# Kernel tuning notes

Hardware: AMD Instinct MI355X
Metric: run time of the kernel (lower is better)

## Reference

```python
import jax, jax.numpy as jnp
import numpy as np
from jax import lax

ANCHOR_AREAS = (128.0**2, 256.0**2, 512.0**2)
ASPECT_RATIOS = (0.5, 1.0, 2.0)
STRIDE = 32.0                      # resnet backbone: get_orig_stat maps fm -> input via x*32
PRE_NMS_TOP_N = 2000
POST_NMS_TOP_N = 100
NMS_IOU_T = 0.7
SCORE_T = 0.1
MIN_SCALE = 0.01
BBOX_XFORM_CLIP = float(np.log(1000.0 / 16.0))


def make_anchors(H, W):
    # anchors laid out in (H, W, A) order to match the offset permutation below
    sizes = []
    for area in ANCHOR_AREAS:
        for r in ASPECT_RATIOS:          # aspect_ratio = w / h
            sizes.append((np.sqrt(area * r), np.sqrt(area / r)))
    sizes = jnp.asarray(np.asarray(sizes, dtype=np.float32))  # [A, 2] (w, h)
    cy = (jnp.arange(H, dtype=jnp.float32) + 0.5) * STRIDE
    cx = (jnp.arange(W, dtype=jnp.float32) + 0.5) * STRIDE
    cyg, cxg = jnp.meshgrid(cy, cx, indexing='ij')             # [H, W]
    cxg = cxg[:, :, None]
    cyg = cyg[:, :, None]
    w = sizes[:, 0]
    h = sizes[:, 1]
    anchors = jnp.stack([cxg - w / 2, cyg - h / 2, cxg + w / 2, cyg + h / 2], axis=-1)
    return anchors.reshape(-1, 4)                              # [H*W*A, 4] xyxy


def decode_boxes(anchors, offsets):
    # anchors [N,4], offsets [B,N,4] (tx, ty, tw, th) -> boxes [B,N,4] xyxy
    wa = anchors[:, 2] - anchors[:, 0]
    ha = anchors[:, 3] - anchors[:, 1]
    cxa = anchors[:, 0] + 0.5 * wa
    cya = anchors[:, 1] + 0.5 * ha
    tx, ty = offsets[..., 0], offsets[..., 1]
    tw = jnp.minimum(offsets[..., 2], BBOX_XFORM_CLIP)
    th = jnp.minimum(offsets[..., 3], BBOX_XFORM_CLIP)
    px = tx * wa + cxa
    py = ty * ha + cya
    pw = jnp.exp(tw) * wa
    ph = jnp.exp(th) * ha
    return jnp.stack([px - pw / 2, py - ph / 2, px + pw / 2, py + ph / 2], axis=-1)


def box_iou(a, b):
    area_a = (a[:, 2] - a[:, 0]) * (a[:, 3] - a[:, 1])
    area_b = (b[:, 2] - b[:, 0]) * (b[:, 3] - b[:, 1])
    lt = jnp.maximum(a[:, None, :2], b[None, :, :2])
    rb = jnp.minimum(a[:, None, 2:], b[None, :, 2:])
    wh = jnp.clip(rb - lt, 0.0)
    inter = wh[..., 0] * wh[..., 1]
    return inter / (area_a[:, None] + area_b[None, :] - inter + 1e-9)


def nms_single(boxes, scores):
    # boxes [P,4] sorted by descending score; invalid entries carry score -1
    P = boxes.shape[0]
    iou = box_iou(boxes, boxes)
    idx = jnp.arange(P)

    def body(i, keep):
        sup = (iou[i] > NMS_IOU_T) & (idx > i)
        return jnp.where(keep[i], keep & (~sup), keep)

    keep = lax.stop_gradient(lax.fori_loop(0, P, body, scores > 0.0))
    kept_scores = jnp.where(keep, scores, -1.0)
    top_s, top_i = lax.top_k(kept_scores, POST_NMS_TOP_N)
    return boxes[top_i], top_s


def rpn_forward(features, W1, b1, W2, b2, W3, b3):
    B, Cin, H, W = features.shape
    A = W3.shape[0]
    # 3x3 sliding conv + ReLU
    t = lax.conv_general_dilated(
        features, W1, window_strides=(1, 1), padding='SAME',
        dimension_numbers=('NCHW', 'OIHW', 'NCHW'))
    t = jax.nn.relu(t + b1[None, :, None, None])
    # 1x1 sibling heads as channel contractions
    offs = jnp.einsum('bchw,oc->bohw', t, W2) + b2[None, :, None, None]   # [B, A*4, H, W]
    logits = jnp.einsum('bchw,oc->bohw', t, W3) + b3[None, :, None, None]  # [B, A, H, W]
    # reorder to per-anchor layout (H, W, A)
    offs = offs.reshape(B, A, 4, H, W).transpose(0, 3, 4, 1, 2).reshape(B, -1, 4)
    scores = jax.nn.sigmoid(logits.transpose(0, 2, 3, 1).reshape(B, -1))  # [B, N]
    anchors = make_anchors(H, W)
    boxes = decode_boxes(anchors, offs)                                    # [B, N, 4]
    # clip to image boundary (handle_cross_boundary_boxes during testing)
    img_w, img_h = W * STRIDE, H * STRIDE
    boxes = jnp.stack([
        jnp.clip(boxes[..., 0], 0.0, img_w),
        jnp.clip(boxes[..., 1], 0.0, img_h),
        jnp.clip(boxes[..., 2], 0.0, img_w),
        jnp.clip(boxes[..., 3], 0.0, img_h)], axis=-1)
    # score-threshold + min-scale filtering
    bw = boxes[..., 2] - boxes[..., 0]
    bh = boxes[..., 3] - boxes[..., 1]
    valid = (scores >= SCORE_T) & (bw > MIN_SCALE * img_w) & (bh > MIN_SCALE * img_h)
    masked = jnp.where(valid, scores, -1.0)
    # pre-NMS top-k, then per-image NMS + post-NMS top-n
    top_s, top_i = lax.top_k(masked, PRE_NMS_TOP_N)                        # [B, P]
    top_boxes = jnp.take_along_axis(boxes, top_i[..., None], axis=1)       # [B, P, 4]
    out_boxes, out_scores = jax.vmap(nms_single)(top_boxes, top_s)
    return out_boxes, out_scores                                           # [B,100,4], [B,100]


def setup_inputs() -> dict:
    key = jax.random.key(0)
    ks = jax.random.split(key, 4)
    B, Cin, H, W = 8, 1024, 50, 50
    A = 9
    C = 512
    return {
        'features': jax.random.normal(ks[0], (B, Cin, H, W), jnp.float32),
        'W1': jax.random.normal(ks[1], (C, Cin, 3, 3), jnp.float32) * 0.01,
        'b1': jnp.zeros((C,), jnp.float32),
        'W2': jax.random.normal(ks[2], (A * 4, C), jnp.float32) * 0.01,
        'b2': jnp.zeros((A * 4,), jnp.float32),
        'W3': jax.random.normal(ks[3], (A, C), jnp.float32) * 0.01,
        'b3': jnp.zeros((A,), jnp.float32),
    }


def reference(features, W1, b1, W2, b2, W3, b3):
    return rpn_forward(features, W1, b1, W2, b2, W3, b3)
```

## Files before the change

kernel.cpp:

```cpp
#include <hip/hip_runtime.h>
#include <cstdint>

#define NB 8
#define CIN 1024
#define HDIM 50
#define WDIM 50
#define COUT 512
#define NA 9
#define NANCH (HDIM*WDIM*NA)
#define PRE_N 2000
#define POST_N 100

typedef __attribute__((ext_vector_type(8))) short bf16x8;
typedef __attribute__((ext_vector_type(4))) float f32x4;
typedef __attribute__((ext_vector_type(16))) float f32x16;
typedef __attribute__((ext_vector_type(8))) unsigned short ushort8v;

constexpr size_t TPLANE    = 20578304;
constexpr size_t OFF_TPH   = 0;
constexpr size_t OFF_TPL   = 20578304;
constexpr size_t OFF_BOXES = 41156608;
constexpr size_t OFF_KEYS  = 44036608;
constexpr size_t OFF_TBOX  = 45476608;
constexpr size_t OFF_TS    = 45732608;
constexpr size_t OFF_SUP   = 45796608;
constexpr size_t QDIM      = 2976;
constexpr size_t PLSTRIDE  = QDIM * 8;
constexpr size_t PPLANE    = 48758784;
constexpr size_t OFF_PH    = 49892864;
constexpr size_t OFF_PL    = OFF_PH + PPLANE;
constexpr size_t WPLANE    = 9437184;
constexpr size_t OFF_WH    = 147410432;
constexpr size_t OFF_WL    = OFF_WH + WPLANE;

__device__ __forceinline__ void split2bf16(float v, unsigned short &hi, unsigned short &lo) {
    unsigned int u = __float_as_uint(v);
    unsigned int r = u + 0x7FFFu + ((u >> 16) & 1u);
    hi = (unsigned short)(r >> 16);
    float hf = __uint_as_float(((unsigned int)hi) << 16);
    float lf = v - hf;
    unsigned int u2 = __float_as_uint(lf);
    unsigned int r2 = u2 + 0x7FFFu + ((u2 >> 16) & 1u);
    lo = (unsigned short)(r2 >> 16);
}

__device__ __forceinline__ void gl_lds(const unsigned short* g, unsigned short* l) {
    __builtin_amdgcn_global_load_lds(
        (const __attribute__((address_space(1))) unsigned int*)(const void*)g,
        (__attribute__((address_space(3))) unsigned int*)(void*)l,
        16, 0, 0);
}

__global__ __launch_bounds__(256) void prep_all(const float* __restrict__ f,
                                                const float* __restrict__ W1,
                                                unsigned short* __restrict__ Ph,
                                                unsigned short* __restrict__ Pl,
                                                unsigned short* __restrict__ Wh,
                                                unsigned short* __restrict__ Wl) {
    int blk = blockIdx.x;
    if (blk < 5952) {
        int id = blk * 256 + threadIdx.x;
        int q = id % (int)QDIM; int r = id / (int)QDIM;
        int cic = r % 64; int b = r / 64;
        int pp = q - 53;
        int rr = pp / 52, cc = pp - rr * 52;
        int h = rr - 1, w = cc - 1;
        bool inb = (pp >= 0) && (pp < 2704) && (h >= 0) && (h < HDIM) && (w >= 0) && (w < WDIM);
        ushort8v hv0, lv0, hv1, lv1;
#pragma unroll
        for (int j = 0; j < 16; ++j) {
            float v = 0.f;
            if (inb) v = f[(((size_t)b * CIN + cic * 16 + j) * HDIM + h) * WDIM + w];
            unsigned short hi, lo;
            split2bf16(v, hi, lo);
            if (j < 8) { hv0[j] = hi; lv0[j] = lo; }
            else       { hv1[j - 8] = hi; lv1[j - 8] = lo; }
        }
        size_t b0 = ((size_t)((b * 64 + cic) * 2 + 0)) * PLSTRIDE + (size_t)q * 8;
        size_t b1 = ((size_t)((b * 64 + cic) * 2 + 1)) * PLSTRIDE + (size_t)q * 8;
        *(ushort8v*)&Ph[b0] = hv0;
        *(ushort8v*)&Ph[b1] = hv1;
        *(ushort8v*)&Pl[b0] = lv0;
        *(ushort8v*)&Pl[b1] = lv1;
    } else {
        int id = (blk - 5952) * 256 + threadIdx.x;
        int co = id % 64; int r = id / 64;
        int cic = r % 64; int cot = r / 64;
        int cog = cot * 64 + co;
        const float* src = W1 + ((size_t)cog * CIN + cic * 16) * 9;
        float v[144];
#pragma unroll
        for (int i = 0; i < 36; ++i) {
            float4 x = ((const float4*)src)[i];
            v[i * 4 + 0] = x.x; v[i * 4 + 1] = x.y; v[i * 4 + 2] = x.z; v[i * 4 + 3] = x.w;
        }
#pragma unroll
        for (int tap = 0; tap < 9; ++tap) {
            ushort8v hv0, lv0, hv1, lv1;
#pragma unroll
            for (int j = 0; j < 16; ++j) {
                unsigned short hi, lo;
                split2bf16(v[j * 9 + tap], hi, lo);
                if (j < 8) { hv0[j] = hi; lv0[j] = lo; }
                else       { hv1[j - 8] = hi; lv1[j - 8] = lo; }
            }
            size_t base = (((size_t)(cot * 64 + cic) * 9 + tap) * 2) * 512;
            *(ushort8v*)&Wh[base + co * 8]       = hv0;
            *(ushort8v*)&Wh[base + 512 + co * 8] = hv1;
            *(ushort8v*)&Wl[base + co * 8]       = lv0;
            *(ushort8v*)&Wl[base + 512 + co * 8] = lv1;
        }
    }
}

__global__ __launch_bounds__(256, 2) void conv_mfma(const unsigned short* __restrict__ FPh,
                                                    const unsigned short* __restrict__ FPl,
                                                    const unsigned short* __restrict__ WPh,
                                                    const unsigned short* __restrict__ WPl,
                                                    const float* __restrict__ b1,
                                                    unsigned short* __restrict__ Tph,
                                                    unsigned short* __restrict__ Tpl) {
    __shared__ unsigned short sA[2][2][3072];
    __shared__ unsigned short sB[2][9216];

    int blk = blockIdx.x;
    int cot = blk & 7;
    int ptile = (blk >> 3) % 11;
    int b = blk / 88;
    int co0 = cot * 64;
    int P0 = 32 + ptile * 256;

    int t = threadIdx.x, wv = t >> 6, ln = t & 63;
    int lm = ln & 31, lk = ln >> 5;

    f32x16 acc[2][2];
#pragma unroll
    for (int jm = 0; jm < 2; ++jm)
#pragma unroll
        for (int jn = 0; jn < 2; ++jn)
#pragma unroll
            for (int rg = 0; rg < 16; ++rg) acc[jm][jn][rg] = 0.f;

#pragma unroll 1
    for (int cic = 0; cic < 64; ++cic) {
        __syncthreads();
#pragma unroll
        for (int k = 0; k < 15; ++k) {
            int id = wv * 15 + k;
            if (id < 24) {
                int hl = id / 12, lkc = (id / 6) & 1, s = id % 6;
                const unsigned short* pl = hl ? FPl : FPh;
                const unsigned short* src = pl
                    + ((size_t)((b * 64 + cic) * 2 + lkc)) * PLSTRIDE
                    + (size_t)P0 * 8 + s * 512 + ln * 8;
                gl_lds(src, &sA[hl][lkc][s * 512]);
            } else {
                int j = id - 24;
                int hl = j / 18, s = j % 18;
                const unsigned short* pl = hl ? WPl : WPh;
                const unsigned short* src = pl + (size_t)(cot * 64 + cic) * 9216 + s * 512 + ln * 8;
                gl_lds(src, &sB[hl][s * 512]);
            }
        }
        __syncthreads();

#pragma unroll
        for (int tap = 0; tap < 9; ++tap) {
            const int kh = tap / 3, kw = tap % 3;
            const int dlt = (kh - 1) * 52 + (kw - 1);
            bf16x8 a[2][2], bb[2][2];
#pragma unroll
            for (int jm = 0; jm < 2; ++jm) {
                int e = (wv * 2 + jm) * 32 + lm + dlt + 53;
                int ad = e * 8;
                a[jm][0] = *(const bf16x8*)&sA[0][lk][ad];
                a[jm][1] = *(const bf16x8*)&sA[1][lk][ad];
            }
#pragma unroll
            for (int jn = 0; jn < 2; ++jn) {
                int bd = tap * 1024 + lk * 512 + (jn * 32 + lm) * 8;
                bb[jn][0] = *(const bf16x8*)&sB[0][bd];
                bb[jn][1] = *(const bf16x8*)&sB[1][bd];
            }
#pragma unroll
            for (int jm = 0; jm < 2; ++jm)
#pragma unroll
                for (int jn = 0; jn < 2; ++jn) {
                    acc[jm][jn] = __builtin_amdgcn_mfma_f32_32x32x16_bf16(a[jm][0], bb[jn][0], acc[jm][jn], 0, 0, 0);
                    acc[jm][jn] = __builtin_amdgcn_mfma_f32_32x32x16_bf16(a[jm][0], bb[jn][1], acc[jm][jn], 0, 0, 0);
                    acc[jm][jn] = __builtin_amdgcn_mfma_f32_32x32x16_bf16(a[jm][1], bb[jn][0], acc[jm][jn], 0, 0, 0);
                }
        }
    }

#pragma unroll
    for (int jn = 0; jn < 2; ++jn) {
        int co = co0 + jn * 32 + lm;
        float bv = b1[co];
#pragma unroll
        for (int jm = 0; jm < 2; ++jm) {
#pragma unroll
            for (int rg = 0; rg < 16; ++rg) {
                int mrow = (rg & 3) + 8 * (rg >> 2) + 4 * lk;
                int pp = P0 + (wv * 2 + jm) * 32 + mrow;
                int rr = pp / 52, cc = pp - rr * 52;
                int h = rr - 1, w = cc - 1;
                if ((unsigned)h < HDIM && (unsigned)w < WDIM) {
                    float v = fmaxf(acc[jm][jn][rg] + bv, 0.f);
                    unsigned short hi, lo;
                    split2bf16(v, hi, lo);
                    int px = b * 2500 + h * 50 + w;
                    size_t sa = (((((size_t)(px >> 7) * 16 + (co >> 5)) * 8 + ((px >> 4) & 7)) * 4
                                  + ((co >> 3) & 3)) * 16 + (px & 15)) * 8 + (co & 7);
                    Tph[sa] = hi;
                    Tpl[sa] = lo;
                }
            }
        }
    }
}

__global__ __launch_bounds__(256) void proj_decode_mfma(const unsigned short* __restrict__ Tph,
                                                        const unsigned short* __restrict__ Tpl,
                                                        const float* __restrict__ W2,
                                                        const float* __restrict__ b2,
                                                        const float* __restrict__ W3,
                                                        const float* __restrict__ b3,
                                                        float* __restrict__ boxes,
                                                        unsigned long long* __restrict__ keys) {
    __shared__ unsigned short sTh[4096], sTl[4096];
    __shared__ unsigned short sWh[1536], sWl[1536];
    __shared__ float pout[128 * 46];

    int blk = blockIdx.x;
    int px0 = blk * 128;
    int t = threadIdx.x, wv = t >> 6, ln = t & 63;
    int lm = ln & 15, q = ln >> 4;

    f32x4 acc[2][3];
#pragma unroll
    for (int jm = 0; jm < 2; ++jm)
#pragma unroll
        for (int nf = 0; nf < 3; ++nf) acc[jm][nf] = (f32x4){0.f, 0.f, 0.f, 0.f};

#pragma unroll 1
    for (int cc16 = 0; cc16 < 16; ++cc16) {
        __syncthreads();
        size_t base = ((size_t)blk * 16 + cc16) * 4096;
        if (wv == 0) {
#pragma unroll
            for (int s = 0; s < 4; ++s) gl_lds(Tph + base + s * 512 + ln * 8, &sTh[s * 512]);
        } else if (wv == 1) {
#pragma unroll
            for (int s = 4; s < 8; ++s) gl_lds(Tph + base + s * 512 + ln * 8, &sTh[s * 512]);
        } else if (wv == 2) {
#pragma unroll
            for (int s = 0; s < 4; ++s) gl_lds(Tpl + base + s * 512 + ln * 8, &sTl[s * 512]);
        } else {
#pragma unroll
            for (int s = 4; s < 8; ++s) gl_lds(Tpl + base + s * 512 + ln * 8, &sTl[s * 512]);
        }
        int c0 = cc16 * 32;
        for (int idx = t; idx < 1536; idx += 256) {
            int o = idx >> 5, ci = idx & 31;
            float v = 0.f;
            if (o < 36) v = W2[o * 512 + c0 + ci];
            else if (o < 45) v = W3[(o - 36) * 512 + c0 + ci];
            unsigned short hi, lo;
            split2bf16(v, hi, lo);
            int ad = (((o >> 4) * 4 + (ci >> 3)) * 16 + (o & 15)) * 8 + (ci & 7);
            sWh[ad] = hi; sWl[ad] = lo;
        }
        __syncthreads();

        bf16x8 a[2][2], bb[3][2];
#pragma unroll
        for (int jm = 0; jm < 2; ++jm) {
            int mf = wv * 2 + jm;
            int ad = ((mf * 4 + q) * 16 + lm) * 8;
            a[jm][0] = *(const bf16x8*)&sTh[ad];
            a[jm][1] = *(const bf16x8*)&sTl[ad];
        }
#pragma unroll
        for (int nf = 0; nf < 3; ++nf) {
            int ad = ((nf * 4 + q) * 16 + lm) * 8;
            bb[nf][0] = *(const bf16x8*)&sWh[ad];
            bb[nf][1] = *(const bf16x8*)&sWl[ad];
        }
#pragma unroll
        for (int jm = 0; jm < 2; ++jm)
#pragma unroll
            for (int nf = 0; nf < 3; ++nf) {
                acc[jm][nf] = __builtin_amdgcn_mfma_f32_16x16x32_bf16(a[jm][0], bb[nf][0], acc[jm][nf], 0, 0, 0);
                acc[jm][nf] = __builtin_amdgcn_mfma_f32_16x16x32_bf16(a[jm][0], bb[nf][1], acc[jm][nf], 0, 0, 0);
                acc[jm][nf] = __builtin_amdgcn_mfma_f32_16x16x32_bf16(a[jm][1], bb[nf][0], acc[jm][nf], 0, 0, 0);
            }
    }
    __syncthreads();
#pragma unroll
    for (int jm = 0; jm < 2; ++jm)
#pragma unroll
        for (int nf = 0; nf < 3; ++nf) {
            int o = nf * 16 + lm;
            if (o < 45) {
                float bias = (o < 36) ? b2[o] : b3[o - 36];
#pragma unroll
                for (int rg = 0; rg < 4; ++rg) {
                    int pxl = (wv * 2 + jm) * 16 + q * 4 + rg;
                    pout[pxl * 46 + o] = acc[jm][nf][rg] + bias;
                }
            }
        }
    __syncthreads();

    const float AW[9] = {90.50966799187809f, 128.0f, 181.01933598375618f,
                         181.01933598375618f, 256.0f, 362.03867196751236f,
                         362.03867196751236f, 512.0f, 724.0773439350247f};
    const float AH[9] = {181.01933598375618f, 128.0f, 90.50966799187809f,
                         362.03867196751236f, 256.0f, 181.01933598375618f,
                         724.0773439350247f, 512.0f, 362.03867196751236f};
    const float CLIPV = 4.135166556742356f;
    const float IMG = 1600.0f;

    for (int it = t; it < 128 * 9; it += 256) {
        int pxl = it / 9, a = it - pxl * 9;
        int pxg = px0 + pxl;
        if (pxg >= 20000) continue;
        int b = pxg / 2500, rem = pxg % 2500;
        int h = rem / 50, w = rem % 50;

        float tx = pout[pxl * 46 + a * 4 + 0];
        float ty = pout[pxl * 46 + a * 4 + 1];
        float tw = pout[pxl * 46 + a * 4 + 2];
        float th = pout[pxl * 46 + a * 4 + 3];
        float lg = pout[pxl * 46 + 36 + a];

        float s = 1.0f / (1.0f + expf(-lg));

        float cx = ((float)w + 0.5f) * 32.0f;
        float cy = ((float)h + 0.5f) * 32.0f;
        float x1a = cx - 0.5f * AW[a];
        float x2a = cx + 0.5f * AW[a];
        float y1a = cy - 0.5f * AH[a];
        float y2a = cy + 0.5f * AH[a];
        float waf = x2a - x1a;
        float haf = y2a - y1a;
        float cxa = x1a + 0.5f * waf;
        float cya = y1a + 0.5f * haf;

        float twc = tw < CLIPV ? tw : CLIPV;
        float thc = th < CLIPV ? th : CLIPV;
        float pxc = tx * waf + cxa;
        float pyc = ty * haf + cya;
        float pw  = expf(twc) * waf;
        float ph  = expf(thc) * haf;

        float x1 = pxc - 0.5f * pw;
        float y1 = pyc - 0.5f * ph;
        float x2 = pxc + 0.5f * pw;
        float y2 = pyc + 0.5f * ph;
        x1 = fminf(fmaxf(x1, 0.f), IMG);
        y1 = fminf(fmaxf(y1, 0.f), IMG);
        x2 = fminf(fmaxf(x2, 0.f), IMG);
        y2 = fminf(fmaxf(y2, 0.f), IMG);

        float bw = x2 - x1, bh = y2 - y1;
        bool valid = (s >= 0.1f) && (bw > 16.0f) && (bh > 16.0f);
        float m = valid ? s : -1.0f;

        int idx = (h * WDIM + w) * NA + a;
        size_t gi = (size_t)b * NANCH + idx;
        ((float4*)boxes)[gi] = make_float4(x1, y1, x2, y2);
        unsigned int u = __float_as_uint(m);
        unsigned int k32 = (u & 0x80000000u) ? ~u : (u | 0x80000000u);
        keys[gi] = ((unsigned long long)k32 << 15) | (unsigned long long)(32767 - idx);
    }
}

__global__ __launch_bounds__(1024) void select_sort_kernel(const unsigned long long* __restrict__ keys,
                                                           const float* __restrict__ boxes,
                                                           float* __restrict__ top_boxes,
                                                           float* __restrict__ top_s) {
    int b = blockIdx.x;
    int t = threadIdx.x;
    int wv = t >> 6;
    const unsigned long long* kb = keys + (size_t)b * NANCH;

    __shared__ unsigned int whist[16][256];
    __shared__ unsigned int hist[256];
    __shared__ int s_chosen, s_rnew;
    __shared__ unsigned int s_cnt;
    __shared__ unsigned long long skeys[2048];

    const int widths[6] = {8, 8, 8, 8, 8, 7};
    unsigned long long prefix = 0;
    int bitsdone = 0;
    int r = PRE_N;

    for (int p = 0; p < 6; ++p) {
        int width = widths[p];
        int bins = 1 << width;
        int shift = 47 - bitsdone - width;
        for (int i = t; i < 16 * 256; i += 1024) ((unsigned int*)whist)[i] = 0;
        __syncthreads();
        for (int i = t; i < NANCH; i += 1024) {
            unsigned long long k = kb[i];
            if ((k >> (47 - bitsdone)) == prefix)
                atomicAdd(&whist[wv][(unsigned)((k >> shift) & (unsigned long long)(bins - 1))], 1u);
        }
        __syncthreads();
        if (t < bins) {
            unsigned int s = 0;
#pragma unroll
            for (int w = 0; w < 16; ++w) s += whist[w][t];
            hist[t] = s;
        }
        __syncthreads();
        if (t == 0) {
            int acc = 0, chosen = 0, rnew = 1;
            for (int d = bins - 1; d >= 0; --d) {
                int hv = (int)hist[d];
                if (acc + hv >= r) { chosen = d; rnew = r - acc; break; }
                acc += hv;
            }
            s_chosen = chosen;
            s_rnew = rnew;
        }
        __syncthreads();
        prefix = (prefix << width) | (unsigned long long)s_chosen;
        bitsdone += width;
        r = s_rnew;
        __syncthreads();
    }
    unsigned long long Kst = prefix;

    if (t == 0) s_cnt = 0;
    __syncthreads();
    for (int i = t; i < NANCH; i += 1024) {
        unsigned long long k = kb[i];
        if (k >= Kst) {
            unsigned int p = atomicAdd(&s_cnt, 1u);
            if (p < 2048) skeys[p] = k;
        }
    }
    __syncthreads();
    unsigned int cnt = s_cnt;
    for (int i = t; i < 2048; i += 1024)
        if (i >= (int)cnt) skeys[i] = 0ull;
    for (int k = 2; k <= 2048; k <<= 1) {
        for (int j = k >> 1; j > 0; j >>= 1) {
            __syncthreads();
            for (int i = t; i < 2048; i += 1024) {
                int l = i ^ j;
                if (l > i) {
                    unsigned long long a = skeys[i], c = skeys[l];
                    bool up = ((i & k) == 0);
                    if (up ? (a < c) : (a > c)) { skeys[i] = c; skeys[l] = a; }
                }
            }
        }
    }
    __syncthreads();
    for (int i = t; i < PRE_N; i += 1024) {
        unsigned long long k = skeys[i];
        unsigned int k32 = (unsigned int)(k >> 15);
        float m = (k32 & 0x80000000u) ? __uint_as_float(k32 & 0x7FFFFFFFu)
                                      : __uint_as_float(~k32);
        unsigned int idx = 32767u - (unsigned int)(k & 32767ull);
        size_t gi = (size_t)b * NANCH + idx;
        top_s[b * PRE_N + i] = m;
        ((float4*)top_boxes)[b * PRE_N + i] = ((const float4*)boxes)[gi];
    }
}

__global__ __launch_bounds__(256) void sup_kernel(const float* __restrict__ top_boxes,
                                                  unsigned long long* __restrict__ supm) {
    int blk = blockIdx.x;
    int b = blk / 125;
    int chunk = blk % 125;
    int t = threadIdx.x;

    __shared__ float bx1[PRE_N], by1[PRE_N], bx2[PRE_N], by2[PRE_N];
    for (int i = t; i < PRE_N; i += 256) {
        float4 v = ((const float4*)top_boxes)[b * PRE_N + i];
        bx1[i] = v.x; by1[i] = v.y; bx2[i] = v.z; by2[i] = v.w;
    }
    __syncthreads();

    int wave = t >> 6, lane = t & 63;
    for (int rr = 0; rr < 4; ++rr) {
        int i = chunk * 16 + wave * 4 + rr;
        float ax1 = bx1[i], ay1 = by1[i], ax2 = bx2[i], ay2 = by2[i];
        float aarea = (ax2 - ax1) * (ay2 - ay1);
        for (int jw = 0; jw < 32; ++jw) {
            int j = jw * 64 + lane;
            bool sup = false;
            if (j > i && j < PRE_N) {
                float jx1 = bx1[j], jy1 = by1[j], jx2 = bx2[j], jy2 = by2[j];
                float ix1 = fmaxf(ax1, jx1), iy1 = fmaxf(ay1, jy1);
                float ix2 = fminf(ax2, jx2), iy2 = fminf(ay2, jy2);
                float iw = fmaxf(ix2 - ix1, 0.f);
                float ih = fmaxf(iy2 - iy1, 0.f);
                float inter = iw * ih;
                float barea = (jx2 - jx1) * (jy2 - jy1);
                float iou = inter / (aarea + barea - inter + 1e-9f);
                sup = iou > 0.7f;
            }
            unsigned long long m = __ballot(sup);
            if (lane == 0) supm[((size_t)b * PRE_N + i) * 32 + jw] = m;
        }
    }
}

__global__ __launch_bounds__(256) void nms_fin_kernel(const float* __restrict__ top_s,
                                                      const unsigned long long* __restrict__ supm,
                                                      const float* __restrict__ top_boxes,
                                                      float* __restrict__ out) {
    int b = blockIdx.x;
    int t = threadIdx.x;
    __shared__ unsigned int kw[64];
    __shared__ int wpre[65];

    if (t < 64) {
        int lane = t;
        unsigned int alive = 0;
        for (int q = 0; q < 32; ++q) {
            int i = lane * 32 + q;
            if (i < PRE_N && top_s[b * PRE_N + i] > 0.f) alive |= (1u << q);
        }
        const unsigned long long* sm = supm + (size_t)b * PRE_N * 32;
        const unsigned int* sup32 = (const unsigned int*)sm;

        for (int tt = 0; tt < 32; ++tt) {
            unsigned int alo = __shfl(alive, 2 * tt);
            unsigned int ahi = __shfl(alive, 2 * tt + 1);
            unsigned long long talive = (unsigned long long)alo | ((unsigned long long)ahi << 32);
            int i_row = tt * 64 + lane;
            unsigned long long rm = (i_row < PRE_N) ? sm[(size_t)i_row * 32 + tt] : 0ull;

            unsigned long long kept = 0, rem = talive;
            while (rem) {
                int j = __builtin_ctzll(rem);
                kept |= (1ull << j);
                unsigned long long rmj = __shfl(rm, j);
                rem &= ~rmj;
                rem &= ~(1ull << j);
            }

            unsigned int oracc = 0;
            unsigned long long kk = kept;
            while (kk) {
                int j0 = __builtin_ctzll(kk); kk &= kk - 1;
                int j1 = -1, j2 = -1, j3 = -1;
                if (kk) { j1 = __builtin_ctzll(kk); kk &= kk - 1; }
                if (kk) { j2 = __builtin_ctzll(kk); kk &= kk - 1; }
                if (kk) { j3 = __builtin_ctzll(kk); kk &= kk - 1; }
                unsigned int v0 = sup32[(size_t)(tt * 64 + j0) * 64 + lane];
                unsigned int v1 = (j1 >= 0) ? sup32[(size_t)(tt * 64 + j1) * 64 + lane] : 0u;
                unsigned int v2 = (j2 >= 0) ? sup32[(size_t)(tt * 64 + j2) * 64 + lane] : 0u;
                unsigned int v3 = (j3 >= 0) ? sup32[(size_t)(tt * 64 + j3) * 64 + lane] : 0u;
                oracc |= v0 | v1 | v2 | v3;
            }
            alive &= ~oracc;
            if (lane == 2 * tt)     alive = (unsigned int)kept;
            if (lane == 2 * tt + 1) alive = (unsigned int)(kept >> 32);
        }
        kw[lane] = alive;
    }
    __syncthreads();
    if (t == 0) {
        int run = 0;
        for (int w = 0; w < 64; ++w) { wpre[w] = run; run += __popc(kw[w]); }
        wpre[64] = run;
    }
    __syncthreads();
    int total = wpre[64];
    float* out_boxes  = out;
    float* out_scores = out + NB * POST_N * 4;
    for (int i = t; i < PRE_N; i += 256) {
        unsigned int w = kw[i >> 5];
        bool kept = (w >> (i & 31)) & 1u;
        int rk = wpre[i >> 5] + __popc(w & ((1u << (i & 31)) - 1u));
        int pos = kept ? rk : total + (i - rk);
        if (pos < POST_N) {
            out_scores[b * POST_N + pos] = kept ? top_s[b * PRE_N + i] : -1.0f;
            ((float4*)out_boxes)[b * POST_N + pos] = ((const float4*)top_boxes)[b * PRE_N + i];
        }
    }
}

extern "C" void kernel_launch(void* const* d_in, const int* in_sizes, int n_in,
                              void* d_out, int out_size, void* d_ws, size_t ws_size,
                              hipStream_t stream) {
    const float* features = (const float*)d_in[0];
    const float* W1 = (const float*)d_in[1];
    const float* b1 = (const float*)d_in[2];
    const float* W2 = (const float*)d_in[3];
    const float* b2 = (const float*)d_in[4];
    const float* W3 = (const float*)d_in[5];
    const float* b3 = (const float*)d_in[6];
    float* out = (float*)d_out;
    char* ws = (char*)d_ws;

    unsigned short* Tph = (unsigned short*)(ws + OFF_TPH);
    unsigned short* Tpl = (unsigned short*)(ws + OFF_TPL);
    float* boxes   = (float*)(ws + OFF_BOXES);
    unsigned long long* keys = (unsigned long long*)(ws + OFF_KEYS);
    float* top_boxes = (float*)(ws + OFF_TBOX);
    float* top_s     = (float*)(ws + OFF_TS);
    unsigned long long* supm = (unsigned long long*)(ws + OFF_SUP);
    unsigned short* FPh = (unsigned short*)(ws + OFF_PH);
    unsigned short* FPl = (unsigned short*)(ws + OFF_PL);
    unsigned short* WPh = (unsigned short*)(ws + OFF_WH);
    unsigned short* WPl = (unsigned short*)(ws + OFF_WL);

    prep_all<<<6080, 256, 0, stream>>>(features, W1, FPh, FPl, WPh, WPl);
    conv_mfma<<<704, 256, 0, stream>>>(FPh, FPl, WPh, WPl, b1, Tph, Tpl);
    proj_decode_mfma<<<157, 256, 0, stream>>>(Tph, Tpl, W2, b2, W3, b3, boxes, keys);
    select_sort_kernel<<<NB, 1024, 0, stream>>>(keys, boxes, top_boxes, top_s);
    sup_kernel<<<NB * 125, 256, 0, stream>>>(top_boxes, supm);
    nms_fin_kernel<<<NB, 256, 0, stream>>>(top_s, supm, top_boxes, out);
}
```

Before: 1.116 ms.

## Double-buffer conv shared-memory tiles to overlap global loads with MFMA compute

The conv kernel now keeps two shared-memory stages in dynamic LDS (120 KB total) and prefetches the next input-channel chunk while computing the current one, which removes one barrier per iteration. It also remaps block indices so that blocks sharing a batch/pixel tile are spread across the launch order. The larger LDS footprint and launch_bounds change cut occupancy to one block per CU, which may limit latency hiding elsewhere.

```diff
diff --git a/kernel.cpp b/kernel.cpp
--- a/kernel.cpp
+++ b/kernel.cpp
@@ -113,20 +113,20 @@
     }
 }
 
-__global__ __launch_bounds__(256, 2) void conv_mfma(const unsigned short* __restrict__ FPh,
+__global__ __launch_bounds__(256, 1) void conv_mfma(const unsigned short* __restrict__ FPh,
                                                     const unsigned short* __restrict__ FPl,
                                                     const unsigned short* __restrict__ WPh,
                                                     const unsigned short* __restrict__ WPl,
                                                     const float* __restrict__ b1,
                                                     unsigned short* __restrict__ Tph,
                                                     unsigned short* __restrict__ Tpl) {
-    __shared__ unsigned short sA[2][2][3072];
-    __shared__ unsigned short sB[2][9216];
+    extern __shared__ unsigned short smem[];
 
     int blk = blockIdx.x;
-    int cot = blk & 7;
-    int ptile = (blk >> 3) % 11;
-    int b = blk / 88;
+    int logical = (blk & 7) * 88 + (blk >> 3);
+    int cot = logical & 7;
+    int ptile = (logical >> 3) % 11;
+    int b = logical / 88;
     int co0 = cot * 64;
     int P0 = 32 + ptile * 256;
 
@@ -141,9 +141,9 @@
 #pragma unroll
             for (int rg = 0; rg < 16; ++rg) acc[jm][jn][rg] = 0.f;
 
-#pragma unroll 1
-    for (int cic = 0; cic < 64; ++cic) {
-        __syncthreads();
+    auto stage = [&](int cur, int cic) {
+        unsigned short* bA = smem + cur * 30720;
+        unsigned short* bB = bA + 12288;
 #pragma unroll
         for (int k = 0; k < 15; ++k) {
             int id = wv * 15 + k;
@@ -153,17 +153,20 @@
                 const unsigned short* src = pl
                     + ((size_t)((b * 64 + cic) * 2 + lkc)) * PLSTRIDE
                     + (size_t)P0 * 8 + s * 512 + ln * 8;
-                gl_lds(src, &sA[hl][lkc][s * 512]);
+                gl_lds(src, &bA[(hl * 2 + lkc) * 3072 + s * 512]);
             } else {
                 int j = id - 24;
                 int hl = j / 18, s = j % 18;
                 const unsigned short* pl = hl ? WPl : WPh;
                 const unsigned short* src = pl + (size_t)(cot * 64 + cic) * 9216 + s * 512 + ln * 8;
-                gl_lds(src, &sB[hl][s * 512]);
-            }
-        }
-        __syncthreads();
-
+                gl_lds(src, &bB[hl * 9216 + s * 512]);
+            }
+        }
+    };
+
+    auto compute = [&](int cur) {
+        const unsigned short* bA = smem + cur * 30720;
+        const unsigned short* bB = bA + 12288;
 #pragma unroll
         for (int tap = 0; tap < 9; ++tap) {
             const int kh = tap / 3, kw = tap % 3;
@@ -173,14 +176,14 @@
             for (int jm = 0; jm < 2; ++jm) {
                 int e = (wv * 2 + jm) * 32 + lm + dlt + 53;
                 int ad = e * 8;
-                a[jm][0] = *(const bf16x8*)&sA[0][lk][ad];
-                a[jm][1] = *(const bf16x8*)&sA[1][lk][ad];
+                a[jm][0] = *(const bf16x8*)&bA[(0 * 2 + lk) * 3072 + ad];
+                a[jm][1] = *(const bf16x8*)&bA[(1 * 2 + lk) * 3072 + ad];
             }
 #pragma unroll
             for (int jn = 0; jn < 2; ++jn) {
                 int bd = tap * 1024 + lk * 512 + (jn * 32 + lm) * 8;
-                bb[jn][0] = *(const bf16x8*)&sB[0][bd];
-                bb[jn][1] = *(const bf16x8*)&sB[1][bd];
+                bb[jn][0] = *(const bf16x8*)&bB[0 * 9216 + bd];
+                bb[jn][1] = *(const bf16x8*)&bB[1 * 9216 + bd];
             }
 #pragma unroll
             for (int jm = 0; jm < 2; ++jm)
@@ -191,6 +194,19 @@
                     acc[jm][jn] = __builtin_amdgcn_mfma_f32_32x32x16_bf16(a[jm][1], bb[jn][0], acc[jm][jn], 0, 0, 0);
                 }
         }
+    };
+
+    stage(0, 0);
+    __syncthreads();
+
+#pragma unroll 1
+    for (int cc = 0; cc < 32; ++cc) {
+        stage(1, 2 * cc + 1);
+        compute(0);
+        __syncthreads();
+        if (cc < 31) stage(0, 2 * cc + 2);
+        compute(1);
+        __syncthreads();
     }
 
 #pragma unroll
@@ -614,8 +630,15 @@
     unsigned short* WPh = (unsigned short*)(ws + OFF_WH);
     unsigned short* WPl = (unsigned short*)(ws + OFF_WL);
 
+    static bool conv_attr_set = false;
+    if (!conv_attr_set) {
+        hipFuncSetAttribute(reinterpret_cast<const void*>(&conv_mfma),
+                            hipFuncAttributeMaxDynamicSharedMemorySize, 122880);
+        conv_attr_set = true;
+    }
+
     prep_all<<<6080, 256, 0, stream>>>(features, W1, FPh, FPl, WPh, WPl);
-    conv_mfma<<<704, 256, 0, stream>>>(FPh, FPl, WPh, WPl, b1, Tph, Tpl);
+    conv_mfma<<<704, 256, 122880, stream>>>(FPh, FPl, WPh, WPl, b1, Tph, Tpl);
     proj_decode_mfma<<<157, 256, 0, stream>>>(Tph, Tpl, W2, b2, W3, b3, boxes, keys);
     select_sort_kernel<<<NB, 1024, 0, stream>>>(keys, boxes, top_boxes, top_s);
     sup_kernel<<<NB * 125, 256, 0, stream>>>(top_boxes, supm);
```

Measured after the change: 1.124 ms. Within noise of the previous version (+0.6%).

## Double-buffer activation tiles in LDS and stream weights directly from global

Applied to the files above, without the earlier changes.

The conv kernel now double-buffers only the activation tile in LDS, prefetching the next input-channel chunk while computing the current one. Weights are no longer staged in LDS; each wave loads its B fragments straight from global memory, three taps at a time. Launch bounds rise to 3 blocks per SM, blocks are remapped so neighbouring block IDs share weight tiles, and MFMA sections get raised wave priority. This trades one barrier per iteration and less LDS use for more global or L2 traffic on weights and higher register pressure.

```diff
diff --git a/kernel.cpp b/kernel.cpp
--- a/kernel.cpp
+++ b/kernel.cpp
@@ -113,20 +113,20 @@
     }
 }
 
-__global__ __launch_bounds__(256, 2) void conv_mfma(const unsigned short* __restrict__ FPh,
+__global__ __launch_bounds__(256, 3) void conv_mfma(const unsigned short* __restrict__ FPh,
                                                     const unsigned short* __restrict__ FPl,
                                                     const unsigned short* __restrict__ WPh,
                                                     const unsigned short* __restrict__ WPl,
                                                     const float* __restrict__ b1,
                                                     unsigned short* __restrict__ Tph,
                                                     unsigned short* __restrict__ Tpl) {
-    __shared__ unsigned short sA[2][2][3072];
-    __shared__ unsigned short sB[2][9216];
+    __shared__ unsigned short sA[2][4][3072];
 
     int blk = blockIdx.x;
-    int cot = blk & 7;
-    int ptile = (blk >> 3) % 11;
-    int b = blk / 88;
+    int logical = (blk & 7) * 88 + (blk >> 3);
+    int cot = logical & 7;
+    int ptile = (logical >> 3) % 11;
+    int b = logical / 88;
     int co0 = cot * 64;
     int P0 = 32 + ptile * 256;
 
@@ -141,56 +141,62 @@
 #pragma unroll
             for (int rg = 0; rg < 16; ++rg) acc[jm][jn][rg] = 0.f;
 
+    auto stageA = [&](int buf, int cic) {
+#pragma unroll
+        for (int k = 0; k < 6; ++k) {
+            int ac = wv * 6 + k;
+            int hl = ac / 12, lkc = (ac / 6) & 1, s = ac % 6;
+            const unsigned short* pl = hl ? FPl : FPh;
+            const unsigned short* src = pl
+                + ((size_t)((b * 64 + cic) * 2 + lkc)) * PLSTRIDE
+                + (size_t)P0 * 8 + s * 512 + ln * 8;
+            gl_lds(src, &sA[buf][hl * 2 + lkc][s * 512]);
+        }
+    };
+
+    stageA(0, 0);
+    __syncthreads();
+
 #pragma unroll 1
     for (int cic = 0; cic < 64; ++cic) {
-        __syncthreads();
-#pragma unroll
-        for (int k = 0; k < 15; ++k) {
-            int id = wv * 15 + k;
-            if (id < 24) {
-                int hl = id / 12, lkc = (id / 6) & 1, s = id % 6;
-                const unsigned short* pl = hl ? FPl : FPh;
-                const unsigned short* src = pl
-                    + ((size_t)((b * 64 + cic) * 2 + lkc)) * PLSTRIDE
-                    + (size_t)P0 * 8 + s * 512 + ln * 8;
-                gl_lds(src, &sA[hl][lkc][s * 512]);
-            } else {
-                int j = id - 24;
-                int hl = j / 18, s = j % 18;
-                const unsigned short* pl = hl ? WPl : WPh;
-                const unsigned short* src = pl + (size_t)(cot * 64 + cic) * 9216 + s * 512 + ln * 8;
-                gl_lds(src, &sB[hl][s * 512]);
-            }
-        }
-        __syncthreads();
-
-#pragma unroll
-        for (int tap = 0; tap < 9; ++tap) {
-            const int kh = tap / 3, kw = tap % 3;
-            const int dlt = (kh - 1) * 52 + (kw - 1);
-            bf16x8 a[2][2], bb[2][2];
-#pragma unroll
-            for (int jm = 0; jm < 2; ++jm) {
-                int e = (wv * 2 + jm) * 32 + lm + dlt + 53;
-                int ad = e * 8;
-                a[jm][0] = *(const bf16x8*)&sA[0][lk][ad];
-                a[jm][1] = *(const bf16x8*)&sA[1][lk][ad];
-            }
-#pragma unroll
-            for (int jn = 0; jn < 2; ++jn) {
-                int bd = tap * 1024 + lk * 512 + (jn * 32 + lm) * 8;
-                bb[jn][0] = *(const bf16x8*)&sB[0][bd];
-                bb[jn][1] = *(const bf16x8*)&sB[1][bd];
-            }
-#pragma unroll
-            for (int jm = 0; jm < 2; ++jm)
+        int abuf = cic & 1;
+        size_t woff = (size_t)(cot * 64 + cic) * 9216;
+#pragma unroll
+        for (int tg = 0; tg < 3; ++tg) {
+            bf16x8 bb[3][2][2];
+#pragma unroll
+            for (int tl = 0; tl < 3; ++tl)
 #pragma unroll
                 for (int jn = 0; jn < 2; ++jn) {
-                    acc[jm][jn] = __builtin_amdgcn_mfma_f32_32x32x16_bf16(a[jm][0], bb[jn][0], acc[jm][jn], 0, 0, 0);
-                    acc[jm][jn] = __builtin_amdgcn_mfma_f32_32x32x16_bf16(a[jm][0], bb[jn][1], acc[jm][jn], 0, 0, 0);
-                    acc[jm][jn] = __builtin_amdgcn_mfma_f32_32x32x16_bf16(a[jm][1], bb[jn][0], acc[jm][jn], 0, 0, 0);
+                    size_t o = woff + (size_t)((tg * 3 + tl) * 1024 + lk * 512 + (jn * 32 + lm) * 8);
+                    bb[tl][jn][0] = *(const bf16x8*)&WPh[o];
+                    bb[tl][jn][1] = *(const bf16x8*)&WPl[o];
                 }
-        }
+            if (tg == 0 && cic + 1 < 64) stageA(abuf ^ 1, cic + 1);
+
+            __builtin_amdgcn_s_setprio(1);
+#pragma unroll
+            for (int tl = 0; tl < 3; ++tl) {
+                const int dlt = (tg - 1) * 52 + (tl - 1);
+                bf16x8 a[2][2];
+#pragma unroll
+                for (int jm = 0; jm < 2; ++jm) {
+                    int ad = ((wv * 2 + jm) * 32 + lm + dlt + 53) * 8;
+                    a[jm][0] = *(const bf16x8*)&sA[abuf][lk][ad];
+                    a[jm][1] = *(const bf16x8*)&sA[abuf][2 + lk][ad];
+                }
+#pragma unroll
+                for (int jm = 0; jm < 2; ++jm)
+#pragma unroll
+                    for (int jn = 0; jn < 2; ++jn) {
+                        acc[jm][jn] = __builtin_amdgcn_mfma_f32_32x32x16_bf16(a[jm][0], bb[tl][jn][0], acc[jm][jn], 0, 0, 0);
+                        acc[jm][jn] = __builtin_amdgcn_mfma_f32_32x32x16_bf16(a[jm][0], bb[tl][jn][1], acc[jm][jn], 0, 0, 0);
+                        acc[jm][jn] = __builtin_amdgcn_mfma_f32_32x32x16_bf16(a[jm][1], bb[tl][jn][0], acc[jm][jn], 0, 0, 0);
+                    }
+            }
+            __builtin_amdgcn_s_setprio(0);
+        }
+        __syncthreads();
     }
 
 #pragma unroll
```

Result: no change. 1.118 ms (+0.1%).
